# Performance work log

Measured on AMD Instinct MI355X. Metric: run time of the kernel, lower is better.

The kernel has to match this reference:

```python
import jax, jax.numpy as jnp
import numpy as np
import math

WIN = 8
N = WIN * WIN          # window_area = 64
H = 6                  # num_heads
DH = 32                # head_dim = dim // num_heads
DIM = 192
B_ = 8192              # batch * num_windows
LOG_MAX = math.log(1.0 / 0.01)
EPS = 1e-12            # F.normalize eps


def _checkerboard_mask():
    wm = np.ones((WIN, WIN))
    wm[0::2, 1::2] = 0
    wm[1::2, 0::2] = 0
    f = wm.reshape(-1)
    return jnp.asarray(np.outer(f, f).astype(bool))  # [N, N], True = keep


def _rel_pos_index():
    coords = np.stack(np.meshgrid(np.arange(WIN), np.arange(WIN), indexing='ij'))
    cf = coords.reshape(2, -1)
    rel = (cf[:, :, None] - cf[:, None, :]).transpose(1, 2, 0).copy()
    rel[:, :, 0] += WIN - 1
    rel[:, :, 1] += WIN - 1
    rel[:, :, 0] *= 2 * WIN - 1
    return rel.sum(-1).astype(np.int32)  # [N, N] in [0, 224]


def setup_inputs() -> dict:
    key = jax.random.key(0)
    ks = jax.random.split(key, 5)
    return {
        'x': jax.random.normal(ks[0], (B_, N, DIM), jnp.float32),
        'qkv_w': jax.random.normal(ks[1], (3 * H * DH, DIM), jnp.float32) * 0.02,
        'qkv_b': jnp.zeros((3 * H * DH,), jnp.float32),
        'proj_w': jax.random.normal(ks[2], (DIM, H * DH), jnp.float32) * 0.02,
        'proj_b': jnp.zeros((DIM,), jnp.float32),
        'logit_scale': jnp.full((H, 1, 1), math.log(10.0), jnp.float32),
        'rel_bias_table': jax.random.normal(ks[3], ((2 * WIN - 1) ** 2, H), jnp.float32) * 0.02,
        'rel_pos_index': jnp.asarray(_rel_pos_index()),
    }


def _l2norm(t):
    n = jnp.linalg.norm(t, axis=-1, keepdims=True)
    return t / jnp.maximum(n, EPS)


def reference(x, qkv_w, qkv_b, proj_w, proj_b, logit_scale, rel_bias_table, rel_pos_index):
    B = x.shape[0]
    # qkv projection -> [3, B, H, N, DH]
    qkv = (jnp.einsum('bnc,oc->bno', x, qkv_w) + qkv_b)
    qkv = qkv.reshape(B, N, 3, H, DH).transpose(2, 0, 3, 1, 4)
    q, k, v = qkv[0], qkv[1], qkv[2]

    # cosine-similarity attention logits
    attn = jnp.einsum('bhnd,bhmd->bhnm', _l2norm(q), _l2norm(k))
    scale = jnp.exp(jnp.minimum(logit_scale, LOG_MAX))  # [H,1,1]
    attn = attn * scale[None]

    # relative position bias: gather [N*N,H] -> [1,H,N,N]
    bias = rel_bias_table[rel_pos_index.reshape(-1)].reshape(N, N, H).transpose(2, 0, 1)
    attn = attn + bias[None]

    # checkerboard mask + softmax with fully-masked-row (NaN) fixup -> zeros
    cb = _checkerboard_mask()[None, None]  # [1,1,N,N]
    neg = jnp.where(cb, attn, -jnp.inf)
    m = jnp.max(neg, axis=-1, keepdims=True)
    m_safe = jnp.where(jnp.isfinite(m), m, 0.0)
    e = jnp.where(cb, jnp.exp(neg - m_safe), 0.0)
    s = jnp.sum(e, axis=-1, keepdims=True)
    p = jnp.where(s > 0, e / jnp.where(s > 0, s, 1.0), 0.0)

    out = jnp.einsum('bhnm,bhmd->bhnd', p, v)
    out = out.transpose(0, 2, 1, 3).reshape(B, N, H * DH)
    return jnp.einsum('bnd,od->bno', out, proj_w) + proj_b
```

## Files before the change

kernel.cpp:

```cpp
#include <hip/hip_runtime.h>

typedef _Float16 h8 __attribute__((ext_vector_type(8)));
typedef _Float16 h2 __attribute__((ext_vector_type(2)));
typedef float f4 __attribute__((ext_vector_type(4)));

#define NHEADS 6
#define LOGMAX 4.6051701859880914f

__device__ __forceinline__ int S_of(int j) { return ((j >> 2) << 3) + ((j & 3) << 1) + ((j >> 2) & 1); }
__device__ __forceinline__ int SC_of(int j) { return ((j >> 2) << 3) + ((j & 3) << 1) + (1 - ((j >> 2) & 1)); }

template <int CTRL>
__device__ __forceinline__ float dpp_mov(float x) {
    return __builtin_bit_cast(float,
        __builtin_amdgcn_update_dpp(0, __builtin_bit_cast(int, x), CTRL, 0xF, 0xF, true));
}
__device__ __forceinline__ float rowsum16(float x) {
    x += dpp_mov<0x121>(x);
    x += dpp_mov<0x122>(x);
    x += dpp_mov<0x124>(x);
    x += dpp_mov<0x128>(x);
    return x;
}
__device__ __forceinline__ float rowmax16(float x) {
    x = fmaxf(x, dpp_mov<0x121>(x));
    x = fmaxf(x, dpp_mov<0x122>(x));
    x = fmaxf(x, dpp_mov<0x124>(x));
    x = fmaxf(x, dpp_mov<0x128>(x));
    return x;
}
__device__ __forceinline__ unsigned pack2(float a, float b) {
    h2 v; v[0] = (_Float16)a; v[1] = (_Float16)b;
    return __builtin_bit_cast(unsigned, v);
}

__global__ void pack_kernel(const float* __restrict__ qkv_w,
                            const float* __restrict__ proj_w,
                            const float* __restrict__ rel_bias_table,
                            const int* __restrict__ rel_pos_index,
                            _Float16* __restrict__ qkvp,
                            _Float16* __restrict__ projp,
                            float* __restrict__ biask) {
    int tid = blockIdx.x * 256 + threadIdx.x;
    const int NQ = 6 * 6 * 6 * 64;
    const int NP = 6 * 12 * 64;
    if (tid < NQ) {
        int l = tid & 63;
        int rest = tid >> 6;
        int ks = rest % 6;
        int nt = (rest / 6) % 6;
        int h = rest / 36;
        int o = (nt >> 1) * 192 + h * 32 + (nt & 1) * 16 + (l & 15);
        int k0 = ks * 32 + (l >> 4) * 8;
        const float* src = qkv_w + o * 192 + k0;
        _Float16* dst = qkvp + tid * 8;
#pragma unroll
        for (int j = 0; j < 8; ++j) dst[j] = (_Float16)src[j];
    } else if (tid < NQ + NP) {
        int t = tid - NQ;
        int l = t & 63;
        int rest = t >> 6;
        int nt = rest % 12;
        int h = rest / 12;
        int o = nt * 16 + (l & 15);
        const float* srcrow = proj_w + o * 192 + h * 32;
        _Float16* dst = projp + t * 8;
        int p0 = (l >> 4) * 8;
#pragma unroll
        for (int j = 0; j < 8; ++j) {
            int p = p0 + j;
            dst[j] = (_Float16)srcrow[(p >> 1) + ((p & 1) << 4)];
        }
    } else if (tid < NQ + NP + 6 * 32 * 32) {
        int t = tid - (NQ + NP);
        int h = t >> 10;
        int jr = (t >> 5) & 31;
        int ic = t & 31;
        int rp = rel_pos_index[S_of(jr) * 64 + S_of(ic)];
        biask[t] = rel_bias_table[rp * NHEADS + h];
    }
}

__global__ __launch_bounds__(128) __attribute__((amdgpu_waves_per_eu(4, 8)))
void cwa_kernel(
    const float* __restrict__ x,
    const _Float16* __restrict__ qkvp,
    const _Float16* __restrict__ projp,
    const float* __restrict__ biask,
    const float* __restrict__ qkv_b,
    const float* __restrict__ proj_b,
    const float* __restrict__ logit_scale,
    float* __restrict__ out) {
    __shared__ __align__(16) unsigned knu[32][20];
    __shared__ __align__(16) _Float16 vT[32][40];
    __shared__ __align__(16) unsigned tmpu[2][16][20];
    __shared__ __align__(16) unsigned outSu[32][100];

    const int tid = threadIdx.x;
    const int lane = tid & 63;
    const int mh = tid >> 6;
    const int cl = lane & 15;
    const int g = lane >> 4;
    const long w0 = blockIdx.x;

    {
        int rowi = tid >> 2;
        int sub = tid & 3;
        long base = (w0 * 64 + SC_of(rowi)) * 192;
#pragma unroll
        for (int i = 0; i < 12; ++i) {
            int c4 = i * 4 + sub;
            *(f4*)(out + base + c4 * 4) = *(const f4*)(proj_b + c4 * 4);
        }
    }

    h8 xf[6];
    {
        long xbase = (w0 * 64 + S_of(mh * 16 + cl)) * 192;
#pragma unroll
        for (int ks = 0; ks < 6; ++ks) {
            f4 u0 = *(const f4*)(x + xbase + ks * 32 + g * 8);
            f4 u1 = *(const f4*)(x + xbase + ks * 32 + g * 8 + 4);
            h8 hv;
            hv[0] = (_Float16)u0[0]; hv[1] = (_Float16)u0[1];
            hv[2] = (_Float16)u0[2]; hv[3] = (_Float16)u0[3];
            hv[4] = (_Float16)u1[0]; hv[5] = (_Float16)u1[1];
            hv[6] = (_Float16)u1[2]; hv[7] = (_Float16)u1[3];
            xf[ks] = hv;
        }
    }

#pragma unroll 1
    for (int h = 0; h < NHEADS; ++h) {
        const _Float16* qb_h = qkvp + (long)h * 6 * 6 * 64 * 8;

        f4 acc[6];
#pragma unroll
        for (int nt = 0; nt < 6; ++nt) acc[nt] = 0.0f;
#pragma unroll
        for (int ks = 0; ks < 6; ++ks) {
#pragma unroll
            for (int nt = 0; nt < 6; ++nt) {
                h8 b = *(const h8*)(qb_h + (((nt * 6 + ks) * 64 + lane) << 3));
                acc[nt] = __builtin_amdgcn_mfma_f32_16x16x32_f16(xf[ks], b, acc[nt], 0, 0, 0);
            }
        }
        float bq0 = qkv_b[h * 32 + cl], bq1 = qkv_b[h * 32 + 16 + cl];
        float bk0 = qkv_b[192 + h * 32 + cl], bk1 = qkv_b[192 + h * 32 + 16 + cl];
        float bv0 = qkv_b[384 + h * 32 + cl], bv1 = qkv_b[384 + h * 32 + 16 + cl];
        unsigned qw[4], kw[4];
        float vv0[4], vv1[4];
#pragma unroll
        for (int r = 0; r < 4; ++r) {
            float t0 = acc[0][r] + bq0, t1 = acc[1][r] + bq1;
            float ss = rowsum16(t0 * t0 + t1 * t1);
            float rs = 1.0f / fmaxf(sqrtf(ss), 1e-12f);
            qw[r] = pack2(t0 * rs, t1 * rs);
            t0 = acc[2][r] + bk0; t1 = acc[3][r] + bk1;
            ss = rowsum16(t0 * t0 + t1 * t1);
            rs = 1.0f / fmaxf(sqrtf(ss), 1e-12f);
            kw[r] = pack2(t0 * rs, t1 * rs);
            vv0[r] = acc[4][r] + bv0;
            vv1[r] = acc[5][r] + bv1;
        }
        __syncthreads();
#pragma unroll
        for (int r = 0; r < 4; ++r) {
            int q = g * 4 + r;
            tmpu[mh][q][cl] = qw[r];
            knu[mh * 16 + q][cl] = kw[r];
            int kvpos = 2 * q + mh;
            vT[cl][kvpos] = (_Float16)vv0[r];
            vT[16 + cl][kvpos] = (_Float16)vv1[r];
        }
        __syncthreads();

        {
            h8 aq = *(const h8*)(&tmpu[mh][cl][g * 4]);
            f4 sN[2];
            sN[0] = 0.0f; sN[1] = 0.0f;
#pragma unroll
            for (int nt = 0; nt < 2; ++nt) {
                h8 bk_ = *(const h8*)(&knu[nt * 16 + cl][g * 4]);
                sN[nt] = __builtin_amdgcn_mfma_f32_16x16x32_f16(aq, bk_, sN[nt], 0, 0, 0);
            }
            float scale = __expf(fminf(logit_scale[h], LOGMAX));
            float lg[2][4];
#pragma unroll
            for (int nt = 0; nt < 2; ++nt)
#pragma unroll
                for (int r = 0; r < 4; ++r)
                    lg[nt][r] = sN[nt][r] * scale +
                                biask[h * 1024 + (mh * 16 + g * 4 + r) * 32 + nt * 16 + cl];
            unsigned pw[4];
#pragma unroll
            for (int r = 0; r < 4; ++r) {
                float mx = rowmax16(fmaxf(lg[0][r], lg[1][r]));
                float e0 = __expf(lg[0][r] - mx);
                float e1 = __expf(lg[1][r] - mx);
                float inv = 1.0f / rowsum16(e0 + e1);
                pw[r] = pack2(e0 * inv, e1 * inv);
            }
#pragma unroll
            for (int r = 0; r < 4; ++r)
                tmpu[mh][g * 4 + r][cl] = pw[r];
            h8 ap = *(const h8*)(&tmpu[mh][cl][g * 4]);
            f4 ov[2];
            ov[0] = 0.0f; ov[1] = 0.0f;
#pragma unroll
            for (int nt = 0; nt < 2; ++nt) {
                h8 bv_ = *(const h8*)(&vT[nt * 16 + cl][g * 8]);
                ov[nt] = __builtin_amdgcn_mfma_f32_16x16x32_f16(ap, bv_, ov[nt], 0, 0, 0);
            }
#pragma unroll
            for (int r = 0; r < 4; ++r)
                outSu[mh * 16 + g * 4 + r][h * 16 + cl] = pack2(ov[0][r], ov[1][r]);
        }
    }
    __syncthreads();

    {
        const int wn = mh;
        const int r0 = cl;
        const int r1 = 16 + cl;
#pragma unroll 1
        for (int pass = 0; pass < 2; ++pass) {
            f4 pa0[3], pa1[3];
#pragma unroll
            for (int nt = 0; nt < 3; ++nt) { pa0[nt] = 0.0f; pa1[nt] = 0.0f; }
#pragma unroll
            for (int ks = 0; ks < 6; ++ks) {
                h8 a0 = *(const h8*)(&outSu[r0][ks * 16 + g * 4]);
                h8 a1 = *(const h8*)(&outSu[r1][ks * 16 + g * 4]);
#pragma unroll
                for (int nt = 0; nt < 3; ++nt) {
                    int ntg = wn * 6 + pass * 3 + nt;
                    h8 b = *(const h8*)(projp + (((ks * 12 + ntg) * 64 + lane) << 3));
                    pa0[nt] = __builtin_amdgcn_mfma_f32_16x16x32_f16(a0, b, pa0[nt], 0, 0, 0);
                    pa1[nt] = __builtin_amdgcn_mfma_f32_16x16x32_f16(a1, b, pa1[nt], 0, 0, 0);
                }
            }
#pragma unroll
            for (int m = 0; m < 2; ++m) {
                const f4* pm = m ? pa1 : pa0;
#pragma unroll
                for (int r = 0; r < 4; ++r) {
                    int rl = m * 16 + g * 4 + r;
                    long grow = w0 * 64 + S_of(rl);
                    float* po_ = out + grow * 192 + wn * 96 + pass * 48 + cl;
#pragma unroll
                    for (int nt = 0; nt < 3; ++nt)
                        po_[nt * 16] = pm[nt][r] + proj_b[wn * 96 + pass * 48 + nt * 16 + cl];
                }
            }
        }
    }
}

extern "C" void kernel_launch(void* const* d_in, const int* in_sizes, int n_in,
                              void* d_out, int out_size, void* d_ws, size_t ws_size,
                              hipStream_t stream) {
    const float* x = (const float*)d_in[0];
    const float* qkv_w = (const float*)d_in[1];
    const float* qkv_b = (const float*)d_in[2];
    const float* proj_w = (const float*)d_in[3];
    const float* proj_b = (const float*)d_in[4];
    const float* logit_scale = (const float*)d_in[5];
    const float* rel_bias_table = (const float*)d_in[6];
    const int* rel_pos_index = (const int*)d_in[7];
    float* out = (float*)d_out;

    const int B = in_sizes[0] / (64 * 192);

    _Float16* qkvp = (_Float16*)d_ws;
    _Float16* projp = qkvp + 6 * 6 * 6 * 64 * 8;
    float* biask = (float*)(projp + 6 * 12 * 64 * 8);

    pack_kernel<<<96, 256, 0, stream>>>(qkv_w, proj_w, rel_bias_table, rel_pos_index,
                                        qkvp, projp, biask);
    cwa_kernel<<<B, 128, 0, stream>>>(x, qkvp, projp, biask, qkv_b, proj_b,
                                      logit_scale, out);
}
```

Before: 259.3 us.

## Split heads across three waves per window instead of query rows across two

The block grows from two to three waves. Before, each wave owned 16 query rows and all waves walked the six heads together with two block barriers per head. Now each wave owns whole heads (two each) for all 32 rows, which removes the per-head __syncthreads and keeps Q/K/V in wave-private LDS. The output projection is also re-split so each wave computes 64 output columns in one pass. This doubles the x fragments held in registers and triples the per-head LDS buffers, which may reduce occupancy.

```diff
diff --git a/kernel.cpp b/kernel.cpp
--- a/kernel.cpp
+++ b/kernel.cpp
@@ -81,7 +81,7 @@
     }
 }
 
-__global__ __launch_bounds__(128) __attribute__((amdgpu_waves_per_eu(4, 8)))
+__global__ __launch_bounds__(192) __attribute__((amdgpu_waves_per_eu(4, 8)))
 void cwa_kernel(
     const float* __restrict__ x,
     const _Float16* __restrict__ qkvp,
@@ -91,32 +91,28 @@
     const float* __restrict__ proj_b,
     const float* __restrict__ logit_scale,
     float* __restrict__ out) {
-    __shared__ __align__(16) unsigned knu[32][20];
-    __shared__ __align__(16) _Float16 vT[32][40];
-    __shared__ __align__(16) unsigned tmpu[2][16][20];
-    __shared__ __align__(16) unsigned outSu[32][100];
+    __shared__ __align__(16) unsigned tmpu[3][32][16];
+    __shared__ __align__(16) unsigned knu[3][32][16];
+    __shared__ __align__(16) _Float16 vT[3][32][40];
+    __shared__ __align__(16) unsigned outSu[32][96];
 
     const int tid = threadIdx.x;
     const int lane = tid & 63;
-    const int mh = tid >> 6;
+    const int wv = tid >> 6;
     const int cl = lane & 15;
     const int g = lane >> 4;
-    const long w0 = blockIdx.x;
-
-    {
-        int rowi = tid >> 2;
-        int sub = tid & 3;
-        long base = (w0 * 64 + SC_of(rowi)) * 192;
-#pragma unroll
-        for (int i = 0; i < 12; ++i) {
-            int c4 = i * 4 + sub;
-            *(f4*)(out + base + c4 * 4) = *(const f4*)(proj_b + c4 * 4);
-        }
-    }
-
-    h8 xf[6];
-    {
-        long xbase = (w0 * 64 + S_of(mh * 16 + cl)) * 192;
+    const long win = blockIdx.x;
+
+#pragma unroll
+    for (int e = tid, it = 0; it < 8; e += 192, ++it) {
+        int row = e / 48, c4 = e % 48;
+        *(f4*)(out + (win * 64 + SC_of(row)) * 192 + c4 * 4) = *(const f4*)(proj_b + c4 * 4);
+    }
+
+    h8 xf[2][6];
+#pragma unroll
+    for (int mt = 0; mt < 2; ++mt) {
+        long xbase = (win * 64 + S_of(mt * 16 + cl)) * 192;
 #pragma unroll
         for (int ks = 0; ks < 6; ++ks) {
             f4 u0 = *(const f4*)(x + xbase + ks * 32 + g * 8);
@@ -126,134 +122,159 @@
             hv[2] = (_Float16)u0[2]; hv[3] = (_Float16)u0[3];
             hv[4] = (_Float16)u1[0]; hv[5] = (_Float16)u1[1];
             hv[6] = (_Float16)u1[2]; hv[7] = (_Float16)u1[3];
-            xf[ks] = hv;
+            xf[mt][ks] = hv;
         }
     }
 
 #pragma unroll 1
-    for (int h = 0; h < NHEADS; ++h) {
-        const _Float16* qb_h = qkvp + (long)h * 6 * 6 * 64 * 8;
-
-        f4 acc[6];
-#pragma unroll
-        for (int nt = 0; nt < 6; ++nt) acc[nt] = 0.0f;
-#pragma unroll
-        for (int ks = 0; ks < 6; ++ks) {
-#pragma unroll
-            for (int nt = 0; nt < 6; ++nt) {
-                h8 b = *(const h8*)(qb_h + (((nt * 6 + ks) * 64 + lane) << 3));
-                acc[nt] = __builtin_amdgcn_mfma_f32_16x16x32_f16(xf[ks], b, acc[nt], 0, 0, 0);
-            }
-        }
+    for (int hi = 0; hi < 2; ++hi) {
+        const int h = wv + hi * 3;
+        const _Float16* qb_h = qkvp + (long)h * 18432;
+
         float bq0 = qkv_b[h * 32 + cl], bq1 = qkv_b[h * 32 + 16 + cl];
         float bk0 = qkv_b[192 + h * 32 + cl], bk1 = qkv_b[192 + h * 32 + 16 + cl];
         float bv0 = qkv_b[384 + h * 32 + cl], bv1 = qkv_b[384 + h * 32 + 16 + cl];
-        unsigned qw[4], kw[4];
-        float vv0[4], vv1[4];
-#pragma unroll
-        for (int r = 0; r < 4; ++r) {
-            float t0 = acc[0][r] + bq0, t1 = acc[1][r] + bq1;
-            float ss = rowsum16(t0 * t0 + t1 * t1);
-            float rs = 1.0f / fmaxf(sqrtf(ss), 1e-12f);
-            qw[r] = pack2(t0 * rs, t1 * rs);
-            t0 = acc[2][r] + bk0; t1 = acc[3][r] + bk1;
-            ss = rowsum16(t0 * t0 + t1 * t1);
-            rs = 1.0f / fmaxf(sqrtf(ss), 1e-12f);
-            kw[r] = pack2(t0 * rs, t1 * rs);
-            vv0[r] = acc[4][r] + bv0;
-            vv1[r] = acc[5][r] + bv1;
-        }
-        __syncthreads();
-#pragma unroll
-        for (int r = 0; r < 4; ++r) {
-            int q = g * 4 + r;
-            tmpu[mh][q][cl] = qw[r];
-            knu[mh * 16 + q][cl] = kw[r];
-            int kvpos = 2 * q + mh;
-            vT[cl][kvpos] = (_Float16)vv0[r];
-            vT[16 + cl][kvpos] = (_Float16)vv1[r];
-        }
-        __syncthreads();
 
         {
-            h8 aq = *(const h8*)(&tmpu[mh][cl][g * 4]);
-            f4 sN[2];
-            sN[0] = 0.0f; sN[1] = 0.0f;
-#pragma unroll
-            for (int nt = 0; nt < 2; ++nt) {
-                h8 bk_ = *(const h8*)(&knu[nt * 16 + cl][g * 4]);
-                sN[nt] = __builtin_amdgcn_mfma_f32_16x16x32_f16(aq, bk_, sN[nt], 0, 0, 0);
+            f4 acc[2][2];
+            acc[0][0] = 0.0f; acc[0][1] = 0.0f; acc[1][0] = 0.0f; acc[1][1] = 0.0f;
+#pragma unroll
+            for (int ks = 0; ks < 6; ++ks)
+#pragma unroll
+                for (int nt = 0; nt < 2; ++nt) {
+                    h8 b = *(const h8*)(qb_h + (((nt * 6 + ks) * 64 + lane) << 3));
+                    acc[0][nt] = __builtin_amdgcn_mfma_f32_16x16x32_f16(xf[0][ks], b, acc[0][nt], 0, 0, 0);
+                    acc[1][nt] = __builtin_amdgcn_mfma_f32_16x16x32_f16(xf[1][ks], b, acc[1][nt], 0, 0, 0);
+                }
+#pragma unroll
+            for (int mt = 0; mt < 2; ++mt)
+#pragma unroll
+                for (int r = 0; r < 4; ++r) {
+                    float t0 = acc[mt][0][r] + bq0, t1 = acc[mt][1][r] + bq1;
+                    float ss = rowsum16(t0 * t0 + t1 * t1);
+                    float rs = 1.0f / fmaxf(sqrtf(ss), 1e-12f);
+                    tmpu[wv][mt * 16 + g * 4 + r][cl] = pack2(t0 * rs, t1 * rs);
+                }
+        }
+        {
+            f4 acc[2][2];
+            acc[0][0] = 0.0f; acc[0][1] = 0.0f; acc[1][0] = 0.0f; acc[1][1] = 0.0f;
+#pragma unroll
+            for (int ks = 0; ks < 6; ++ks)
+#pragma unroll
+                for (int nt = 0; nt < 2; ++nt) {
+                    h8 b = *(const h8*)(qb_h + ((((nt + 2) * 6 + ks) * 64 + lane) << 3));
+                    acc[0][nt] = __builtin_amdgcn_mfma_f32_16x16x32_f16(xf[0][ks], b, acc[0][nt], 0, 0, 0);
+                    acc[1][nt] = __builtin_amdgcn_mfma_f32_16x16x32_f16(xf[1][ks], b, acc[1][nt], 0, 0, 0);
+                }
+#pragma unroll
+            for (int mt = 0; mt < 2; ++mt)
+#pragma unroll
+                for (int r = 0; r < 4; ++r) {
+                    float t0 = acc[mt][0][r] + bk0, t1 = acc[mt][1][r] + bk1;
+                    float ss = rowsum16(t0 * t0 + t1 * t1);
+                    float rs = 1.0f / fmaxf(sqrtf(ss), 1e-12f);
+                    knu[wv][mt * 16 + g * 4 + r][cl] = pack2(t0 * rs, t1 * rs);
+                }
+        }
+        {
+            f4 acc[2][2];
+            acc[0][0] = 0.0f; acc[0][1] = 0.0f; acc[1][0] = 0.0f; acc[1][1] = 0.0f;
+#pragma unroll
+            for (int ks = 0; ks < 6; ++ks)
+#pragma unroll
+                for (int nt = 0; nt < 2; ++nt) {
+                    h8 b = *(const h8*)(qb_h + ((((nt + 4) * 6 + ks) * 64 + lane) << 3));
+                    acc[0][nt] = __builtin_amdgcn_mfma_f32_16x16x32_f16(xf[0][ks], b, acc[0][nt], 0, 0, 0);
+                    acc[1][nt] = __builtin_amdgcn_mfma_f32_16x16x32_f16(xf[1][ks], b, acc[1][nt], 0, 0, 0);
+                }
+#pragma unroll
+            for (int mt = 0; mt < 2; ++mt)
+#pragma unroll
+                for (int r = 0; r < 4; ++r) {
+                    int pos = 2 * (g * 4 + r) + mt;
+                    vT[wv][cl][pos] = (_Float16)(acc[mt][0][r] + bv0);
+                    vT[wv][16 + cl][pos] = (_Float16)(acc[mt][1][r] + bv1);
+                }
+        }
+
+        {
+            h8 aq0 = *(const h8*)(&tmpu[wv][cl][g * 4]);
+            h8 aq1 = *(const h8*)(&tmpu[wv][16 + cl][g * 4]);
+            h8 bk0_ = *(const h8*)(&knu[wv][cl][g * 4]);
+            h8 bk1_ = *(const h8*)(&knu[wv][16 + cl][g * 4]);
+            f4 s[2][2];
+            s[0][0] = 0.0f; s[0][1] = 0.0f; s[1][0] = 0.0f; s[1][1] = 0.0f;
+            s[0][0] = __builtin_amdgcn_mfma_f32_16x16x32_f16(aq0, bk0_, s[0][0], 0, 0, 0);
+            s[0][1] = __builtin_amdgcn_mfma_f32_16x16x32_f16(aq0, bk1_, s[0][1], 0, 0, 0);
+            s[1][0] = __builtin_amdgcn_mfma_f32_16x16x32_f16(aq1, bk0_, s[1][0], 0, 0, 0);
+            s[1][1] = __builtin_amdgcn_mfma_f32_16x16x32_f16(aq1, bk1_, s[1][1], 0, 0, 0);
+
+            float scale = __expf(fminf(logit_scale[h], LOGMAX));
+#pragma unroll
+            for (int mt = 0; mt < 2; ++mt)
+#pragma unroll
+                for (int r = 0; r < 4; ++r) {
+                    int row = mt * 16 + g * 4 + r;
+                    float lg0 = s[mt][0][r] * scale + biask[h * 1024 + row * 32 + cl];
+                    float lg1 = s[mt][1][r] * scale + biask[h * 1024 + row * 32 + 16 + cl];
+                    float mx = rowmax16(fmaxf(lg0, lg1));
+                    float e0 = __expf(lg0 - mx);
+                    float e1 = __expf(lg1 - mx);
+                    float inv = 1.0f / rowsum16(e0 + e1);
+                    tmpu[wv][row][cl] = pack2(e0 * inv, e1 * inv);
+                }
+
+            h8 ap0 = *(const h8*)(&tmpu[wv][cl][g * 4]);
+            h8 ap1 = *(const h8*)(&tmpu[wv][16 + cl][g * 4]);
+            h8 bv0_ = *(const h8*)(&vT[wv][cl][g * 8]);
+            h8 bv1_ = *(const h8*)(&vT[wv][16 + cl][g * 8]);
+            f4 ov[2][2];
+            ov[0][0] = 0.0f; ov[0][1] = 0.0f; ov[1][0] = 0.0f; ov[1][1] = 0.0f;
+            ov[0][0] = __builtin_amdgcn_mfma_f32_16x16x32_f16(ap0, bv0_, ov[0][0], 0, 0, 0);
+            ov[0][1] = __builtin_amdgcn_mfma_f32_16x16x32_f16(ap0, bv1_, ov[0][1], 0, 0, 0);
+            ov[1][0] = __builtin_amdgcn_mfma_f32_16x16x32_f16(ap1, bv0_, ov[1][0], 0, 0, 0);
+            ov[1][1] = __builtin_amdgcn_mfma_f32_16x16x32_f16(ap1, bv1_, ov[1][1], 0, 0, 0);
+
+#pragma unroll
+            for (int mt = 0; mt < 2; ++mt)
+#pragma unroll
+                for (int r = 0; r < 4; ++r)
+                    outSu[mt * 16 + g * 4 + r][h * 16 + cl] = pack2(ov[mt][0][r], ov[mt][1][r]);
+        }
+    }
+    __syncthreads();
+
+    {
+        f4 pacc[2][4];
+#pragma unroll
+        for (int mt = 0; mt < 2; ++mt)
+#pragma unroll
+            for (int nt = 0; nt < 4; ++nt) pacc[mt][nt] = 0.0f;
+#pragma unroll
+        for (int ks = 0; ks < 6; ++ks) {
+            h8 a0 = *(const h8*)(&outSu[cl][ks * 16 + g * 4]);
+            h8 a1 = *(const h8*)(&outSu[16 + cl][ks * 16 + g * 4]);
+#pragma unroll
+            for (int nt = 0; nt < 4; ++nt) {
+                h8 b = *(const h8*)(projp + (((ks * 12 + wv * 4 + nt) * 64 + lane) << 3));
+                pacc[0][nt] = __builtin_amdgcn_mfma_f32_16x16x32_f16(a0, b, pacc[0][nt], 0, 0, 0);
+                pacc[1][nt] = __builtin_amdgcn_mfma_f32_16x16x32_f16(a1, b, pacc[1][nt], 0, 0, 0);
             }
-            float scale = __expf(fminf(logit_scale[h], LOGMAX));
-            float lg[2][4];
-#pragma unroll
-            for (int nt = 0; nt < 2; ++nt)
-#pragma unroll
-                for (int r = 0; r < 4; ++r)
-                    lg[nt][r] = sN[nt][r] * scale +
-                                biask[h * 1024 + (mh * 16 + g * 4 + r) * 32 + nt * 16 + cl];
-            unsigned pw[4];
+        }
+        float pb[4];
+#pragma unroll
+        for (int nt = 0; nt < 4; ++nt) pb[nt] = proj_b[wv * 64 + nt * 16 + cl];
+#pragma unroll
+        for (int mt = 0; mt < 2; ++mt)
 #pragma unroll
             for (int r = 0; r < 4; ++r) {
-                float mx = rowmax16(fmaxf(lg[0][r], lg[1][r]));
-                float e0 = __expf(lg[0][r] - mx);
-                float e1 = __expf(lg[1][r] - mx);
-                float inv = 1.0f / rowsum16(e0 + e1);
-                pw[r] = pack2(e0 * inv, e1 * inv);
+                long grow = win * 64 + S_of(mt * 16 + g * 4 + r);
+                float* po_ = out + grow * 192 + wv * 64 + cl;
+#pragma unroll
+                for (int nt = 0; nt < 4; ++nt)
+                    po_[nt * 16] = pacc[mt][nt][r] + pb[nt];
             }
-#pragma unroll
-            for (int r = 0; r < 4; ++r)
-                tmpu[mh][g * 4 + r][cl] = pw[r];
-            h8 ap = *(const h8*)(&tmpu[mh][cl][g * 4]);
-            f4 ov[2];
-            ov[0] = 0.0f; ov[1] = 0.0f;
-#pragma unroll
-            for (int nt = 0; nt < 2; ++nt) {
-                h8 bv_ = *(const h8*)(&vT[nt * 16 + cl][g * 8]);
-                ov[nt] = __builtin_amdgcn_mfma_f32_16x16x32_f16(ap, bv_, ov[nt], 0, 0, 0);
-            }
-#pragma unroll
-            for (int r = 0; r < 4; ++r)
-                outSu[mh * 16 + g * 4 + r][h * 16 + cl] = pack2(ov[0][r], ov[1][r]);
-        }
-    }
-    __syncthreads();
-
-    {
-        const int wn = mh;
-        const int r0 = cl;
-        const int r1 = 16 + cl;
-#pragma unroll 1
-        for (int pass = 0; pass < 2; ++pass) {
-            f4 pa0[3], pa1[3];
-#pragma unroll
-            for (int nt = 0; nt < 3; ++nt) { pa0[nt] = 0.0f; pa1[nt] = 0.0f; }
-#pragma unroll
-            for (int ks = 0; ks < 6; ++ks) {
-                h8 a0 = *(const h8*)(&outSu[r0][ks * 16 + g * 4]);
-                h8 a1 = *(const h8*)(&outSu[r1][ks * 16 + g * 4]);
-#pragma unroll
-                for (int nt = 0; nt < 3; ++nt) {
-                    int ntg = wn * 6 + pass * 3 + nt;
-                    h8 b = *(const h8*)(projp + (((ks * 12 + ntg) * 64 + lane) << 3));
-                    pa0[nt] = __builtin_amdgcn_mfma_f32_16x16x32_f16(a0, b, pa0[nt], 0, 0, 0);
-                    pa1[nt] = __builtin_amdgcn_mfma_f32_16x16x32_f16(a1, b, pa1[nt], 0, 0, 0);
-                }
-            }
-#pragma unroll
-            for (int m = 0; m < 2; ++m) {
-                const f4* pm = m ? pa1 : pa0;
-#pragma unroll
-                for (int r = 0; r < 4; ++r) {
-                    int rl = m * 16 + g * 4 + r;
-                    long grow = w0 * 64 + S_of(rl);
-                    float* po_ = out + grow * 192 + wn * 96 + pass * 48 + cl;
-#pragma unroll
-                    for (int nt = 0; nt < 3; ++nt)
-                        po_[nt * 16] = pm[nt][r] + proj_b[wn * 96 + pass * 48 + nt * 16 + cl];
-                }
-            }
-        }
     }
 }
 
@@ -278,6 +299,6 @@
 
     pack_kernel<<<96, 256, 0, stream>>>(qkv_w, proj_w, rel_bias_table, rel_pos_index,
                                         qkvp, projp, biask);
-    cwa_kernel<<<B, 128, 0, stream>>>(x, qkvp, projp, biask, qkv_b, proj_b,
+    cwa_kernel<<<B, 192, 0, stream>>>(x, qkvp, projp, biask, qkv_b, proj_b,
                                       logit_scale, out);
 }
```

Result: slower. 312.6 us (+20.5%).
